# Kernel optimization log

Measured on AMD Instinct MI355X. Metric: run time of the kernel, lower is better.

## Reference

```python
import jax, jax.numpy as jnp
import numpy as np

NODE_DIM = 16
N_VERTS = 54
SEAT_DIM = 4
HIDDEN = 128
N = 16384
EPS = 1e-5


def _layer_norm(x, g, b):
    m = jnp.mean(x, axis=-1, keepdims=True)
    v = jnp.var(x, axis=-1, keepdims=True)
    return (x - m) * jax.lax.rsqrt(v + EPS) * g + b


def setup_inputs() -> dict:
    key = jax.random.key(0)
    ks = jax.random.split(key, 32)
    h = HIDDEN
    mlp_in = h * 3 + 8
    d = {
        "X": jax.random.normal(ks[0], (N, N_VERTS, NODE_DIM), dtype=jnp.float32),
        "A_hat": jax.random.uniform(ks[1], (N_VERTS, N_VERTS), dtype=jnp.float32) / N_VERTS,
        "v1_idx": jax.random.randint(ks[2], (N,), 0, N_VERTS),
        "v2_idx": jax.random.randint(ks[3], (N,), 0, N_VERTS),
        "seat": jax.random.randint(ks[4], (N,), 0, SEAT_DIM),
        # conv layer 0: in NODE_DIM -> h
        "conv0_W": jax.random.normal(ks[5], (NODE_DIM, h), dtype=jnp.float32) * 0.1,
        "conv0_b": jnp.zeros((h,), jnp.float32),
        "ln0_g": jnp.ones((h,), jnp.float32),
        "ln0_b": jnp.zeros((h,), jnp.float32),
        # conv layers 1,2: h -> h
        "conv1_W": jax.random.normal(ks[6], (h, h), dtype=jnp.float32) * 0.05,
        "conv1_b": jnp.zeros((h,), jnp.float32),
        "ln1_g": jnp.ones((h,), jnp.float32),
        "ln1_b": jnp.zeros((h,), jnp.float32),
        "conv2_W": jax.random.normal(ks[7], (h, h), dtype=jnp.float32) * 0.05,
        "conv2_b": jnp.zeros((h,), jnp.float32),
        "ln2_g": jnp.ones((h,), jnp.float32),
        "ln2_b": jnp.zeros((h,), jnp.float32),
        "seat_emb": jax.random.normal(ks[8], (SEAT_DIM + 1, 8), dtype=jnp.float32),
        "mlp_W1": jax.random.normal(ks[9], (mlp_in, 128), dtype=jnp.float32) * 0.05,
        "mlp_b1": jnp.zeros((128,), jnp.float32),
        "mlp_W2": jax.random.normal(ks[10], (128, 64), dtype=jnp.float32) * 0.1,
        "mlp_b2": jnp.zeros((64,), jnp.float32),
        "mlp_W3": jax.random.normal(ks[11], (64, 1), dtype=jnp.float32) * 0.1,
        "mlp_b3": jnp.zeros((1,), jnp.float32),
        # rank head: mlp_in -> 64 -> 1 (sigmoid)
        "rank_W1": jax.random.normal(ks[12], (mlp_in, 64), dtype=jnp.float32) * 0.05,
        "rank_b1": jnp.zeros((64,), jnp.float32),
        "rank_W2": jax.random.normal(ks[13], (64, 1), dtype=jnp.float32) * 0.1,
        "rank_b2": jnp.zeros((1,), jnp.float32),
    }
    return d


def reference(X, A_hat, v1_idx, v2_idx, seat,
              conv0_W, conv0_b, ln0_g, ln0_b,
              conv1_W, conv1_b, ln1_g, ln1_b,
              conv2_W, conv2_b, ln2_g, ln2_b,
              seat_emb,
              mlp_W1, mlp_b1, mlp_W2, mlp_b2, mlp_W3, mlp_b3,
              rank_W1, rank_b1, rank_W2, rank_b2):
    convs = [(conv0_W, conv0_b, ln0_g, ln0_b),
             (conv1_W, conv1_b, ln1_g, ln1_b),
             (conv2_W, conv2_b, ln2_g, ln2_b)]
    H = X  # (N, 54, in_dim)
    for i, (W, b, g, beta) in enumerate(convs):
        HW = jnp.einsum('nvd,dk->nvk', H, W) + b          # linear
        out = jnp.einsum('ij,njk->nik', A_hat, HW)         # adjacency mix
        H_new = jax.nn.relu(_layer_norm(out, g, beta))     # dropout = identity (eval)
        H = H + H_new if i > 0 else H_new
    n = H.shape[0]
    rows = jnp.arange(n)
    v1_emb = H[rows, v1_idx]                               # (N, h)
    v2_emb = H[rows, v2_idx]
    gpool = jnp.mean(H, axis=1)                            # (N, h)
    s_emb = seat_emb[jnp.clip(seat, 0, SEAT_DIM - 1)]      # (N, 8)
    h = jnp.concatenate([v1_emb, v2_emb, gpool, s_emb], axis=-1)
    z = jax.nn.relu(h @ mlp_W1 + mlp_b1)
    z = jax.nn.relu(z @ mlp_W2 + mlp_b2)
    win_logit = z @ mlp_W3 + mlp_b3                        # (N, 1)
    r = jax.nn.relu(h @ rank_W1 + rank_b1)
    rank_pred = jax.nn.sigmoid(r @ rank_W2 + rank_b2)      # (N, 1)
    return (win_logit, rank_pred)
```

## Files before the change

### kernel.cpp

```cpp
#include <hip/hip_runtime.h>
#include <hip/hip_bf16.h>
#include <math.h>


typedef __bf16 bf16x8 __attribute__((ext_vector_type(8)));
typedef float  f32x4  __attribute__((ext_vector_type(4)));
typedef unsigned int u32x4 __attribute__((ext_vector_type(4)));
typedef unsigned int u32x2 __attribute__((ext_vector_type(2)));

#define DEVINL __device__ __forceinline__
#define HROW 400

DEVINL unsigned bfr(float x) {
    unsigned u = __float_as_uint(x);
    return (u + 0x7fffu + ((u >> 16) & 1u)) >> 16;
}
DEVINL unsigned pk2(float a, float b) {
    float2 f; f.x = a; f.y = b;
    __hip_bfloat162 h = __float22bfloat162_rn(f);
    unsigned u;
    __builtin_memcpy(&u, &h, sizeof(u));
    return u;
}
DEVINL unsigned short bf1(float x) {
    return (unsigned short)bfr(x);
}

DEVINL f32x4 MFMA(u32x4 a, u32x4 b, f32x4 c) {
    return __builtin_amdgcn_mfma_f32_16x16x32_bf16(
        __builtin_bit_cast(bf16x8, a), __builtin_bit_cast(bf16x8, b), c, 0, 0, 0);
}

#define TS 36
#define HS 68
DEVINL int TROW(int r) { return r * TS + ((r >> 3) & 1) * 4; }

DEVINL void conv12g(f32x4 (&rg)[8], const unsigned* Hlds,
                    const u32x4* __restrict__ Wp, int w, int g, int c15, int l)
{
    #pragma unroll
    for (int i = 0; i < 8; ++i) rg[i] = (f32x4){0.f, 0.f, 0.f, 0.f};
    #pragma unroll
    for (int ks = 0; ks < 4; ++ks) {
        u32x4 wf0 = Wp[((2 * w + 0) * 4 + ks) * 64 + l];
        u32x4 wf1 = Wp[((2 * w + 1) * 4 + ks) * 64 + l];
        u32x4 hb[4];
        #pragma unroll
        for (int ut = 0; ut < 4; ++ut)
            hb[ut] = *(const u32x4*)&Hlds[(ut * 16 + c15) * HS + ks * 16 + g * 4];
        #pragma unroll
        for (int ut = 0; ut < 4; ++ut) {
            rg[ut]     = MFMA(wf0, hb[ut], rg[ut]);
            rg[4 + ut] = MFMA(wf1, hb[ut], rg[4 + ut]);
        }
    }
}

DEVINL void conv_epi(const f32x4 (&rg)[8], unsigned short* TldsH,
                     const f32x4 (&bb)[2], int w, int g, int c15)
{
    #pragma unroll
    for (int m2 = 0; m2 < 2; ++m2) {
        const int chb = (2 * w + m2) * 16;
        #pragma unroll
        for (int ut = 0; ut < 4; ++ut) {
            const int u = ut * 16 + c15;
            #pragma unroll
            for (int r = 0; r < 4; ++r)
                TldsH[TROW(chb + g * 4 + r) * 2 + u] = bf1(rg[m2 * 4 + ut][r] + bb[m2][r]);
        }
    }
}

DEVINL void do_mix(f32x4 (&rg)[8], const unsigned* Tlds,
                   u32x4 bfA0, u32x4 bfA1, int g, int c15)
{
    #pragma unroll
    for (int mt = 0; mt < 8; ++mt) {
        const int crow = TROW(mt * 16 + c15) + g * 4;
        u32x4 a0 = *(const u32x4*)&Tlds[crow];
        u32x4 a1 = *(const u32x4*)&Tlds[crow + 16];
        f32x4 a = {0.f, 0.f, 0.f, 0.f};
        a = MFMA(a0, bfA0, a);
        a = MFMA(a1, bfA1, a);
        rg[mt] = a;
    }
}

DEVINL void mix_epi(const f32x4 (&rg)[8], float (&Rf)[8][4], unsigned* Hlds,
                    const float* gam, const float* bet, bool resid, bool writeH,
                    int w, int g, int c15)
{
    float s = 0.f, q = 0.f;
    #pragma unroll
    for (int mt = 0; mt < 8; ++mt)
        #pragma unroll
        for (int r = 0; r < 4; ++r) { float x = rg[mt][r]; s += x; q = fmaf(x, x, q); }
    s += __shfl_xor(s, 16); s += __shfl_xor(s, 32);
    q += __shfl_xor(q, 16); q += __shfl_xor(q, 32);
    const float m   = s * (1.f / 128.f);
    const float var = q * (1.f / 128.f) - m * m;
    const float rs  = rsqrtf(var + 1e-5f);
    const int v = w * 16 + c15;
    #pragma unroll
    for (int mt = 0; mt < 8; ++mt) {
        f32x4 gc = *(const f32x4*)&gam[mt * 16 + g * 4];
        f32x4 bc = *(const f32x4*)&bet[mt * 16 + g * 4];
        #pragma unroll
        for (int r = 0; r < 4; ++r) {
            float val = fmaxf((rg[mt][r] - m) * rs * gc[r] + bc[r], 0.f);
            if (resid) val += Rf[mt][r];
            Rf[mt][r] = val;
        }
        if (writeH) {
            u32x2 pr;
            pr[0] = pk2(Rf[mt][0], Rf[mt][1]);
            pr[1] = pk2(Rf[mt][2], Rf[mt][3]);
            *(u32x2*)&Hlds[v * HS + mt * 8 + g * 2] = pr;
        }
    }
}

__global__ __launch_bounds__(256, 4) void gcn_mfma(
    const float* __restrict__ X, const unsigned* __restrict__ AmG,
    const int* __restrict__ v1i, const int* __restrict__ v2i, const int* __restrict__ seat,
    const float* __restrict__ W0, const float* __restrict__ b0v,
    const float* __restrict__ g0v, const float* __restrict__ be0,
    const unsigned* __restrict__ W1G, const float* __restrict__ b1v,
    const float* __restrict__ g1v, const float* __restrict__ be1,
    const unsigned* __restrict__ W2G, const float* __restrict__ b2v,
    const float* __restrict__ g2v, const float* __restrict__ be2,
    const float* __restrict__ semb, float* __restrict__ hws, int spb)
{
    __shared__ unsigned Tlds[128 * TS + 4];
    __shared__ unsigned Hlds[64 * HS];
    __shared__ float    Gb[6][128];
    __shared__ unsigned long long WpS[2];

    float* SmF = (float*)Tlds;

    const int tid = threadIdx.x;
    const int l = tid & 63, w = tid >> 6, g = l >> 4, c15 = l & 15;

    if (tid < 128) {
        const int c = tid;
        Gb[0][c] = g0v[c]; Gb[1][c] = g1v[c]; Gb[2][c] = g2v[c];
        Gb[3][c] = be0[c]; Gb[4][c] = be1[c]; Gb[5][c] = be2[c];
    }
    if (tid == 0) {
        WpS[0] = (unsigned long long)W1G;
        WpS[1] = (unsigned long long)W2G;
    }

    u32x4 W0f[2];
    #pragma unroll
    for (int m2 = 0; m2 < 2; ++m2) {
        const int ch = (2 * w + m2) * 16 + c15;
        unsigned t0[4];
        #pragma unroll
        for (int jj = 0; jj < 4; ++jj) {
            const int k = g * 8 + 2 * jj;
            t0[jj] = (g < 2) ? pk2(W0[k * 128 + ch], W0[(k + 1) * 128 + ch]) : 0u;
        }
        W0f[m2] = (u32x4){t0[0], t0[1], t0[2], t0[3]};
    }
    f32x4 Bv[3][2];
    #pragma unroll
    for (int m2 = 0; m2 < 2; ++m2) {
        const int ch4 = (2 * w + m2) * 16 + g * 4;
        Bv[0][m2] = *(const f32x4*)&b0v[ch4];
        Bv[1][m2] = *(const f32x4*)&b1v[ch4];
        Bv[2][m2] = *(const f32x4*)&b2v[ch4];
    }
    const u32x4* AmG4 = (const u32x4*)AmG;
    u32x4 AmF0 = AmG4[(w * 2 + 0) * 64 + l];
    u32x4 AmF1 = AmG4[(w * 2 + 1) * 64 + l];
    __syncthreads();

    float Rf[8][4];
    f32x4 rg[8];

    #pragma unroll 1
    for (int it = 0; it < spb; ++it) {
        const int n = blockIdx.x + gridDim.x * it;

        const u32x4* W1p = (const u32x4*)(((volatile unsigned long long*)WpS)[0]);
        const u32x4* W2p = (const u32x4*)(((volatile unsigned long long*)WpS)[1]);

        #pragma unroll
        for (int i = 0; i < 8; ++i) rg[i] = (f32x4){0.f, 0.f, 0.f, 0.f};
        #pragma unroll
        for (int ut = 0; ut < 4; ++ut) {
            const int u = ut * 16 + c15;
            u32x4 xb = (u32x4){0u, 0u, 0u, 0u};
            if (g < 2 && u < 54) {
                const f32x4* xp = (const f32x4*)(X + (size_t)n * 864 + u * 16 + g * 8);
                f32x4 f0 = xp[0], f1 = xp[1];
                xb = (u32x4){pk2(f0[0], f0[1]), pk2(f0[2], f0[3]),
                             pk2(f1[0], f1[1]), pk2(f1[2], f1[3])};
            }
            #pragma unroll
            for (int m2 = 0; m2 < 2; ++m2)
                rg[m2 * 4 + ut] = MFMA(W0f[m2], xb, rg[m2 * 4 + ut]);
        }
        conv_epi(rg, (unsigned short*)Tlds, Bv[0], w, g, c15);
        __syncthreads();
        do_mix(rg, Tlds, AmF0, AmF1, g, c15);
        mix_epi(rg, Rf, Hlds, &Gb[0][0], &Gb[3][0], false, true, w, g, c15);
        __syncthreads();

        conv12g(rg, Hlds, W1p, w, g, c15, l);
        conv_epi(rg, (unsigned short*)Tlds, Bv[1], w, g, c15);
        __syncthreads();
        do_mix(rg, Tlds, AmF0, AmF1, g, c15);
        mix_epi(rg, Rf, Hlds, &Gb[1][0], &Gb[4][0], true, true, w, g, c15);
        __syncthreads();

        conv12g(rg, Hlds, W2p, w, g, c15, l);
        conv_epi(rg, (unsigned short*)Tlds, Bv[2], w, g, c15);
        __syncthreads();
        do_mix(rg, Tlds, AmF0, AmF1, g, c15);
        mix_epi(rg, Rf, Hlds, &Gb[2][0], &Gb[5][0], true, true, w, g, c15);
        __syncthreads();

        const int v1 = v1i[n], v2 = v2i[n];
        int st = seat[n];
        st = st < 0 ? 0 : (st > 3 ? 3 : st);
        float* hr = hws + (size_t)n * HROW;
        const int v = w * 16 + c15;

        if (v == v1 || v == v2) {
            #pragma unroll
            for (int mt = 0; mt < 8; ++mt) {
                f32x4 t;
                #pragma unroll
                for (int r = 0; r < 4; ++r) t[r] = Rf[mt][r];
                if (v == v1) *(f32x4*)&hr[mt * 16 + g * 4] = t;
                if (v == v2) *(f32x4*)&hr[128 + mt * 16 + g * 4] = t;
            }
        }

        {
            const int pair = tid & 63;
            const int nv = (w == 3) ? 6 : 16;
            float s0 = 0.f, s1 = 0.f;
            const unsigned* hb = &Hlds[(w * 16) * HS + pair];
            for (int r = 0; r < nv; ++r) {
                const unsigned u = hb[r * HS];
                s0 += __uint_as_float(u << 16);
                s1 += __uint_as_float(u & 0xffff0000u);
            }
            SmF[w * 128 + 2 * pair]     = s0;
            SmF[w * 128 + 2 * pair + 1] = s1;
        }
        __syncthreads();
        if (tid < 128) {
            const float mn = (SmF[tid] + SmF[128 + tid] + SmF[256 + tid] + SmF[384 + tid])
                             * (1.f / 54.f);
            hr[256 + tid] = mn;
        }
        if (tid < 8)       hr[384 + tid] = semb[st * 8 + tid];
        else if (tid < 16) hr[384 + tid] = 0.f;
        __syncthreads();
    }
}

__global__ void head_frag_init(const float* __restrict__ mW1,
                               const float* __restrict__ rW1,
                               const float* __restrict__ mW2,
                               const float* __restrict__ W1t,
                               const float* __restrict__ W2t,
                               const float* __restrict__ Amat,
                               unsigned* __restrict__ W1h, unsigned* __restrict__ W1l,
                               unsigned* __restrict__ R1h, unsigned* __restrict__ W2h,
                               unsigned* __restrict__ W1G, unsigned* __restrict__ W2G,
                               unsigned* __restrict__ AmG)
{
    const int t = blockIdx.x * 256 + threadIdx.x;
    if (t < 13 * 128 * 16) {
        const int j = t & 3, g = (t >> 2) & 3, col = (t >> 4) & 127, ks = t >> 11;
        const int k = ks * 32 + g * 8 + 2 * j;
        const float w0 = (k < 392)     ? mW1[k * 128 + col]       : 0.f;
        const float w1 = (k + 1 < 392) ? mW1[(k + 1) * 128 + col] : 0.f;
        const unsigned h0 = bfr(w0), h1 = bfr(w1);
        const float l0 = w0 - __uint_as_float(h0 << 16);
        const float l1 = w1 - __uint_as_float(h1 << 16);
        const int idx = ((ks * 8 + (col >> 4)) * 64 + g * 16 + (col & 15)) * 4 + j;
        W1h[idx] = h0 | (h1 << 16);
        W1l[idx] = pk2(l0, l1);
    }
    if (t < 13 * 64 * 16) {
        const int j = t & 3, g = (t >> 2) & 3, col = (t >> 4) & 63, ks = t >> 10;
        const int k = ks * 32 + g * 8 + 2 * j;
        const float w0 = (k < 392)     ? rW1[k * 64 + col]       : 0.f;
        const float w1 = (k + 1 < 392) ? rW1[(k + 1) * 64 + col] : 0.f;
        const int idx = ((ks * 4 + (col >> 4)) * 64 + g * 16 + (col & 15)) * 4 + j;
        R1h[idx] = pk2(w0, w1);
    }
    if (t < 4 * 64 * 16) {
        const int j = t & 3, g = (t >> 2) & 3, col = (t >> 4) & 63, ks2 = t >> 10;
        const int k = ks2 * 32 + g * 8 + 2 * j;
        const int idx = ((ks2 * 4 + (col >> 4)) * 64 + g * 16 + (col & 15)) * 4 + j;
        W2h[idx] = pk2(mW2[k * 64 + col], mW2[(k + 1) * 64 + col]);
    }
    if (t < 8 * 4 * 64 * 4) {
        const int j = t & 3, lane = (t >> 2) & 63, ks = (t >> 8) & 3, ct = t >> 10;
        const int g2 = lane >> 4, c15 = lane & 15;
        const int k = ks * 32 + g2 * 8 + 2 * j;
        const int ch = ct * 16 + c15;
        W1G[t] = pk2(W1t[k * 128 + ch], W1t[(k + 1) * 128 + ch]);
        W2G[t] = pk2(W2t[k * 128 + ch], W2t[(k + 1) * 128 + ch]);
    }
    if (t < 2048) {
        const int j = t & 3, lane = (t >> 2) & 63, h = (t >> 8) & 1, wt = t >> 9;
        const int g2 = lane >> 4, cc = lane & 15;
        const int v = wt * 16 + cc;
        const int u = h * 32 + g2 * 8 + 2 * j;
        const float a0 = (v < 54 && u < 54)     ? Amat[v * 54 + u]     : 0.f;
        const float a1 = (v < 54 && u + 1 < 54) ? Amat[v * 54 + u + 1] : 0.f;
        AmG[t] = pk2(a0, a1);
    }
}

__global__ __launch_bounds__(256, 2) void head_mfma(
    const float* __restrict__ hws,
    const unsigned* __restrict__ W1hG, const unsigned* __restrict__ W1lG,
    const unsigned* __restrict__ R1hG, const unsigned* __restrict__ W2hG,
    const float* __restrict__ mb1, const float* __restrict__ mb2,
    const float* __restrict__ mW3, const float* __restrict__ mb3,
    const float* __restrict__ rb1, const float* __restrict__ rW2,
    const float* __restrict__ rb2,
    float* __restrict__ out, int N)
{
    __shared__ u32x4 Zh[16 * 64];

    const int tid = threadIdx.x, l = tid & 63, w = tid >> 6, g = l >> 4, c15 = l & 15;
    const int row = blockIdx.x * 64 + w * 16 + c15;

    const u32x4* W1h4 = (const u32x4*)W1hG;
    const u32x4* W1l4 = (const u32x4*)W1lG;
    const u32x4* R1h4 = (const u32x4*)R1hG;
    const u32x4* W2h4 = (const u32x4*)W2hG;

    f32x4 z1[8], rr[4];
    #pragma unroll
    for (int i = 0; i < 8; ++i) z1[i] = (f32x4){0.f, 0.f, 0.f, 0.f};
    #pragma unroll
    for (int i = 0; i < 4; ++i) rr[i] = (f32x4){0.f, 0.f, 0.f, 0.f};

    #pragma unroll 1
    for (int ks = 0; ks < 13; ++ks) {
        const float* hp = hws + (size_t)row * HROW + ks * 32 + g * 8;
        f32x4 f0 = *(const f32x4*)hp, f1 = *(const f32x4*)(hp + 4);
        float vv[8] = {f0[0], f0[1], f0[2], f0[3], f1[0], f1[1], f1[2], f1[3]};
        unsigned th[4], tl[4];
        #pragma unroll
        for (int jj = 0; jj < 4; ++jj) {
            unsigned ha = bfr(vv[2 * jj]), hb = bfr(vv[2 * jj + 1]);
            th[jj] = ha | (hb << 16);
            tl[jj] = pk2(vv[2 * jj] - __uint_as_float(ha << 16),
                         vv[2 * jj + 1] - __uint_as_float(hb << 16));
        }
        u32x4 ah = (u32x4){th[0], th[1], th[2], th[3]};
        u32x4 al = (u32x4){tl[0], tl[1], tl[2], tl[3]};
        #pragma unroll
        for (int nt = 0; nt < 8; ++nt) {
            u32x4 bh = W1h4[(ks * 8 + nt) * 64 + l];
            u32x4 bl = W1l4[(ks * 8 + nt) * 64 + l];
            f32x4 a = z1[nt];
            a = MFMA(ah, bh, a); a = MFMA(ah, bl, a); a = MFMA(al, bh, a);
            z1[nt] = a;
        }
        #pragma unroll
        for (int nt = 0; nt < 4; ++nt)
            rr[nt] = MFMA(ah, R1h4[(ks * 4 + nt) * 64 + l], rr[nt]);
    }

    float rp[4] = {0.f, 0.f, 0.f, 0.f};
    #pragma unroll
    for (int nt = 0; nt < 4; ++nt) {
        int c = nt * 16 + c15;
        float rb = rb1[c], rw = rW2[c];
        #pragma unroll
        for (int r = 0; r < 4; ++r) rp[r] += fmaxf(rr[nt][r] + rb, 0.f) * rw;
    }
    #pragma unroll
    for (int r = 0; r < 4; ++r) {
        float p = rp[r];
        #pragma unroll
        for (int m = 1; m <= 8; m <<= 1) p += __shfl_xor(p, m);
        if (c15 == 0) {
            int orow = blockIdx.x * 64 + w * 16 + g * 4 + r;
            out[N + orow] = 1.f / (1.f + expf(-(p + rb2[0])));
        }
    }

    {
        unsigned short* zp = (unsigned short*)Zh;
        #pragma unroll
        for (int nt = 0; nt < 8; ++nt) {
            int c = nt * 16 + c15;
            float bb = mb1[c];
            #pragma unroll
            for (int r = 0; r < 4; ++r) {
                float v = fmaxf(z1[nt][r] + bb, 0.f);
                int lanep = ((nt * 2 + (c15 >> 3)) & 3) * 16 + g * 4 + r;
                zp[((w * 4 + (nt >> 1)) * 64 + lanep) * 8 + (c15 & 7)] = (unsigned short)bfr(v);
            }
        }
    }
    __syncthreads();

    f32x4 z2a[4];
    #pragma unroll
    for (int i = 0; i < 4; ++i) z2a[i] = (f32x4){0.f, 0.f, 0.f, 0.f};
    #pragma unroll
    for (int ks2 = 0; ks2 < 4; ++ks2) {
        u32x4 za = Zh[(w * 4 + ks2) * 64 + l];
        #pragma unroll
        for (int nt2 = 0; nt2 < 4; ++nt2)
            z2a[nt2] = MFMA(za, W2h4[(ks2 * 4 + nt2) * 64 + l], z2a[nt2]);
    }
    float wp[4] = {0.f, 0.f, 0.f, 0.f};
    #pragma unroll
    for (int nt2 = 0; nt2 < 4; ++nt2) {
        int c = nt2 * 16 + c15;
        float bb = mb2[c], w3 = mW3[c];
        #pragma unroll
        for (int r = 0; r < 4; ++r) wp[r] += fmaxf(z2a[nt2][r] + bb, 0.f) * w3;
    }
    #pragma unroll
    for (int r = 0; r < 4; ++r) {
        float p = wp[r];
        #pragma unroll
        for (int m = 1; m <= 8; m <<= 1) p += __shfl_xor(p, m);
        if (c15 == 0) {
            int orow = blockIdx.x * 64 + w * 16 + g * 4 + r;
            out[orow] = p + mb3[0];
        }
    }
}

extern "C" void kernel_launch(void* const* d_in, const int* in_sizes, int n_in,
                              void* d_out, int out_size, void* d_ws, size_t ws_size,
                              hipStream_t stream) {
    const float* X        = (const float*)d_in[0];
    const float* A        = (const float*)d_in[1];
    const int*   v1_idx   = (const int*)d_in[2];
    const int*   v2_idx   = (const int*)d_in[3];
    const int*   seat     = (const int*)d_in[4];
    const float* W0       = (const float*)d_in[5];
    const float* b0       = (const float*)d_in[6];
    const float* g0       = (const float*)d_in[7];
    const float* be0      = (const float*)d_in[8];
    const float* W1       = (const float*)d_in[9];
    const float* b1       = (const float*)d_in[10];
    const float* g1       = (const float*)d_in[11];
    const float* be1      = (const float*)d_in[12];
    const float* W2       = (const float*)d_in[13];
    const float* b2       = (const float*)d_in[14];
    const float* g2       = (const float*)d_in[15];
    const float* be2      = (const float*)d_in[16];
    const float* seat_emb = (const float*)d_in[17];
    const float* mW1      = (const float*)d_in[18];
    const float* mb1      = (const float*)d_in[19];
    const float* mW2      = (const float*)d_in[20];
    const float* mb2      = (const float*)d_in[21];
    const float* mW3      = (const float*)d_in[22];
    const float* mb3      = (const float*)d_in[23];
    const float* rW1      = (const float*)d_in[24];
    const float* rb1      = (const float*)d_in[25];
    const float* rW2      = (const float*)d_in[26];
    const float* rb2      = (const float*)d_in[27];

    const int N = in_sizes[2];
    float* out = (float*)d_out;

    float*    hws = (float*)d_ws;
    unsigned* W1h = (unsigned*)((char*)d_ws + (size_t)N * HROW * 4);
    unsigned* W1l = W1h + 26624;
    unsigned* R1h = W1l + 26624;
    unsigned* W2h = R1h + 13312;
    unsigned* W1G = W2h + 4096;
    unsigned* W2G = W1G + 8192;
    unsigned* AmG = W2G + 8192;

    head_frag_init<<<104, 256, 0, stream>>>(mW1, rW1, mW2, W1, W2, A,
                                            W1h, W1l, R1h, W2h, W1G, W2G, AmG);

    const int spb = 8;
    const int gridA = N / spb;
    gcn_mfma<<<gridA, 256, 0, stream>>>(
        X, AmG, v1_idx, v2_idx, seat,
        W0, b0, g0, be0, W1G, b1, g1, be1, W2G, b2, g2, be2,
        seat_emb, hws, spb);

    const int gridB = N / 64;
    head_mfma<<<gridB, 256, 0, stream>>>(
        hws, W1h, W1l, R1h, W2h,
        mb1, mb2, mW3, mb3, rb1, rW2, rb2, out, N);
}
```

Measured before the change: 389.1 us.

## Keep residual in bf16 LDS instead of registers and prepack conv0 weights

Drops the per-thread fp32 residual array Rf[8][4] and instead reads the previous layer's activation back from the bf16 H buffer in LDS for the residual add. The v1/v2 embedding rows are then gathered from LDS. Conv0 weights are prepacked into MFMA fragment layout by the init kernel and loaded each iteration, and biases move to LDS. The T/H padding scheme changes (TROW swizzle removed, HS 68->66). The aim is to cut VGPR pressure and raise occupancy, at the cost of extra LDS traffic, possible bank conflicts, and bf16 rounding of the residual stream, which also feeds the stored embeddings.

```diff
diff --git a/kernel.cpp b/kernel.cpp
--- a/kernel.cpp
+++ b/kernel.cpp
@@ -22,9 +22,9 @@
     __builtin_memcpy(&u, &h, sizeof(u));
     return u;
 }
-DEVINL unsigned short bf1(float x) {
-    return (unsigned short)bfr(x);
-}
+DEVINL unsigned short bf1(float x) { return (unsigned short)bfr(x); }
+DEVINL float lo16(unsigned u) { return __uint_as_float(u << 16); }
+DEVINL float hi16(unsigned u) { return __uint_as_float(u & 0xffff0000u); }
 
 DEVINL f32x4 MFMA(u32x4 a, u32x4 b, f32x4 c) {
     return __builtin_amdgcn_mfma_f32_16x16x32_bf16(
@@ -32,8 +32,7 @@
 }
 
 #define TS 36
-#define HS 68
-DEVINL int TROW(int r) { return r * TS + ((r >> 3) & 1) * 4; }
+#define HS 66
 
 DEVINL void conv12g(f32x4 (&rg)[8], const unsigned* Hlds,
                     const u32x4* __restrict__ Wp, int w, int g, int c15, int l)
@@ -56,18 +55,19 @@
     }
 }
 
-DEVINL void conv_epi(const f32x4 (&rg)[8], unsigned short* TldsH,
-                     const f32x4 (&bb)[2], int w, int g, int c15)
+DEVINL void conv_epi(const f32x4 (&rg)[8], unsigned short* TldsH, const float* bias,
+                     int w, int g, int c15)
 {
     #pragma unroll
     for (int m2 = 0; m2 < 2; ++m2) {
         const int chb = (2 * w + m2) * 16;
+        f32x4 bb = *(const f32x4*)&bias[chb + g * 4];
         #pragma unroll
         for (int ut = 0; ut < 4; ++ut) {
             const int u = ut * 16 + c15;
             #pragma unroll
             for (int r = 0; r < 4; ++r)
-                TldsH[TROW(chb + g * 4 + r) * 2 + u] = bf1(rg[m2 * 4 + ut][r] + bb[m2][r]);
+                TldsH[(chb + g * 4 + r) * (TS * 2) + u] = bf1(rg[m2 * 4 + ut][r] + bb[r]);
         }
     }
 }
@@ -77,7 +77,7 @@
 {
     #pragma unroll
     for (int mt = 0; mt < 8; ++mt) {
-        const int crow = TROW(mt * 16 + c15) + g * 4;
+        const int crow = (mt * 16 + c15) * TS + g * 4;
         u32x4 a0 = *(const u32x4*)&Tlds[crow];
         u32x4 a1 = *(const u32x4*)&Tlds[crow + 16];
         f32x4 a = {0.f, 0.f, 0.f, 0.f};
@@ -87,8 +87,8 @@
     }
 }
 
-DEVINL void mix_epi(const f32x4 (&rg)[8], float (&Rf)[8][4], unsigned* Hlds,
-                    const float* gam, const float* bet, bool resid, bool writeH,
+DEVINL void mix_epi(const f32x4 (&rg)[8], unsigned* Hlds,
+                    const float* gam, const float* bet, bool resid,
                     int w, int g, int c15)
 {
     float s = 0.f, q = 0.f;
@@ -106,25 +106,27 @@
     for (int mt = 0; mt < 8; ++mt) {
         f32x4 gc = *(const f32x4*)&gam[mt * 16 + g * 4];
         f32x4 bc = *(const f32x4*)&bet[mt * 16 + g * 4];
-        #pragma unroll
-        for (int r = 0; r < 4; ++r) {
-            float val = fmaxf((rg[mt][r] - m) * rs * gc[r] + bc[r], 0.f);
-            if (resid) val += Rf[mt][r];
-            Rf[mt][r] = val;
-        }
-        if (writeH) {
-            u32x2 pr;
-            pr[0] = pk2(Rf[mt][0], Rf[mt][1]);
-            pr[1] = pk2(Rf[mt][2], Rf[mt][3]);
-            *(u32x2*)&Hlds[v * HS + mt * 8 + g * 2] = pr;
-        }
+        unsigned* hp = &Hlds[v * HS + mt * 8 + g * 2];
+        float val[4];
+        #pragma unroll
+        for (int r = 0; r < 4; ++r)
+            val[r] = fmaxf((rg[mt][r] - m) * rs * gc[r] + bc[r], 0.f);
+        if (resid) {
+            u32x2 old = *(const u32x2*)hp;
+            val[0] += lo16(old[0]); val[1] += hi16(old[0]);
+            val[2] += lo16(old[1]); val[3] += hi16(old[1]);
+        }
+        u32x2 pr;
+        pr[0] = pk2(val[0], val[1]);
+        pr[1] = pk2(val[2], val[3]);
+        *(u32x2*)hp = pr;
     }
 }
 
 __global__ __launch_bounds__(256, 4) void gcn_mfma(
     const float* __restrict__ X, const unsigned* __restrict__ AmG,
     const int* __restrict__ v1i, const int* __restrict__ v2i, const int* __restrict__ seat,
-    const float* __restrict__ W0, const float* __restrict__ b0v,
+    const unsigned* __restrict__ W0G, const float* __restrict__ b0v,
     const float* __restrict__ g0v, const float* __restrict__ be0,
     const unsigned* __restrict__ W1G, const float* __restrict__ b1v,
     const float* __restrict__ g1v, const float* __restrict__ be1,
@@ -132,10 +134,10 @@
     const float* __restrict__ g2v, const float* __restrict__ be2,
     const float* __restrict__ semb, float* __restrict__ hws, int spb)
 {
-    __shared__ unsigned Tlds[128 * TS + 4];
+    __shared__ unsigned Tlds[128 * TS];
     __shared__ unsigned Hlds[64 * HS];
-    __shared__ float    Gb[6][128];
-    __shared__ unsigned long long WpS[2];
+    __shared__ float    PrmL[9][128];
+    __shared__ unsigned long long WpS[3];
 
     float* SmF = (float*)Tlds;
 
@@ -144,40 +146,20 @@
 
     if (tid < 128) {
         const int c = tid;
-        Gb[0][c] = g0v[c]; Gb[1][c] = g1v[c]; Gb[2][c] = g2v[c];
-        Gb[3][c] = be0[c]; Gb[4][c] = be1[c]; Gb[5][c] = be2[c];
+        PrmL[0][c] = b0v[c]; PrmL[1][c] = b1v[c]; PrmL[2][c] = b2v[c];
+        PrmL[3][c] = g0v[c]; PrmL[4][c] = g1v[c]; PrmL[5][c] = g2v[c];
+        PrmL[6][c] = be0[c]; PrmL[7][c] = be1[c]; PrmL[8][c] = be2[c];
     }
     if (tid == 0) {
         WpS[0] = (unsigned long long)W1G;
         WpS[1] = (unsigned long long)W2G;
-    }
-
-    u32x4 W0f[2];
-    #pragma unroll
-    for (int m2 = 0; m2 < 2; ++m2) {
-        const int ch = (2 * w + m2) * 16 + c15;
-        unsigned t0[4];
-        #pragma unroll
-        for (int jj = 0; jj < 4; ++jj) {
-            const int k = g * 8 + 2 * jj;
-            t0[jj] = (g < 2) ? pk2(W0[k * 128 + ch], W0[(k + 1) * 128 + ch]) : 0u;
-        }
-        W0f[m2] = (u32x4){t0[0], t0[1], t0[2], t0[3]};
-    }
-    f32x4 Bv[3][2];
-    #pragma unroll
-    for (int m2 = 0; m2 < 2; ++m2) {
-        const int ch4 = (2 * w + m2) * 16 + g * 4;
-        Bv[0][m2] = *(const f32x4*)&b0v[ch4];
-        Bv[1][m2] = *(const f32x4*)&b1v[ch4];
-        Bv[2][m2] = *(const f32x4*)&b2v[ch4];
+        WpS[2] = (unsigned long long)W0G;
     }
     const u32x4* AmG4 = (const u32x4*)AmG;
     u32x4 AmF0 = AmG4[(w * 2 + 0) * 64 + l];
     u32x4 AmF1 = AmG4[(w * 2 + 1) * 64 + l];
     __syncthreads();
 
-    float Rf[8][4];
     f32x4 rg[8];
 
     #pragma unroll 1
@@ -186,58 +168,58 @@
 
         const u32x4* W1p = (const u32x4*)(((volatile unsigned long long*)WpS)[0]);
         const u32x4* W2p = (const u32x4*)(((volatile unsigned long long*)WpS)[1]);
-
-        #pragma unroll
-        for (int i = 0; i < 8; ++i) rg[i] = (f32x4){0.f, 0.f, 0.f, 0.f};
-        #pragma unroll
-        for (int ut = 0; ut < 4; ++ut) {
-            const int u = ut * 16 + c15;
-            u32x4 xb = (u32x4){0u, 0u, 0u, 0u};
-            if (g < 2 && u < 54) {
-                const f32x4* xp = (const f32x4*)(X + (size_t)n * 864 + u * 16 + g * 8);
-                f32x4 f0 = xp[0], f1 = xp[1];
-                xb = (u32x4){pk2(f0[0], f0[1]), pk2(f0[2], f0[3]),
-                             pk2(f1[0], f1[1]), pk2(f1[2], f1[3])};
+        const u32x4* W0p = (const u32x4*)(((volatile unsigned long long*)WpS)[2]);
+
+        {
+            u32x4 w0a = W0p[(2 * w + 0) * 64 + l];
+            u32x4 w0b = W0p[(2 * w + 1) * 64 + l];
+            #pragma unroll
+            for (int i = 0; i < 8; ++i) rg[i] = (f32x4){0.f, 0.f, 0.f, 0.f};
+            #pragma unroll
+            for (int ut = 0; ut < 4; ++ut) {
+                const int u = ut * 16 + c15;
+                u32x4 xb = (u32x4){0u, 0u, 0u, 0u};
+                if (g < 2 && u < 54) {
+                    const f32x4* xp = (const f32x4*)(X + (size_t)n * 864 + u * 16 + g * 8);
+                    f32x4 f0 = xp[0], f1 = xp[1];
+                    xb = (u32x4){pk2(f0[0], f0[1]), pk2(f0[2], f0[3]),
+                                 pk2(f1[0], f1[1]), pk2(f1[2], f1[3])};
+                }
+                rg[ut]     = MFMA(w0a, xb, rg[ut]);
+                rg[4 + ut] = MFMA(w0b, xb, rg[4 + ut]);
             }
-            #pragma unroll
-            for (int m2 = 0; m2 < 2; ++m2)
-                rg[m2 * 4 + ut] = MFMA(W0f[m2], xb, rg[m2 * 4 + ut]);
-        }
-        conv_epi(rg, (unsigned short*)Tlds, Bv[0], w, g, c15);
+        }
+        conv_epi(rg, (unsigned short*)Tlds, &PrmL[0][0], w, g, c15);
         __syncthreads();
         do_mix(rg, Tlds, AmF0, AmF1, g, c15);
-        mix_epi(rg, Rf, Hlds, &Gb[0][0], &Gb[3][0], false, true, w, g, c15);
+        mix_epi(rg, Hlds, &PrmL[3][0], &PrmL[6][0], false, w, g, c15);
         __syncthreads();
 
         conv12g(rg, Hlds, W1p, w, g, c15, l);
-        conv_epi(rg, (unsigned short*)Tlds, Bv[1], w, g, c15);
+        conv_epi(rg, (unsigned short*)Tlds, &PrmL[1][0], w, g, c15);
         __syncthreads();
         do_mix(rg, Tlds, AmF0, AmF1, g, c15);
-        mix_epi(rg, Rf, Hlds, &Gb[1][0], &Gb[4][0], true, true, w, g, c15);
+        mix_epi(rg, Hlds, &PrmL[4][0], &PrmL[7][0], true, w, g, c15);
         __syncthreads();
 
         conv12g(rg, Hlds, W2p, w, g, c15, l);
-        conv_epi(rg, (unsigned short*)Tlds, Bv[2], w, g, c15);
+        conv_epi(rg, (unsigned short*)Tlds, &PrmL[2][0], w, g, c15);
         __syncthreads();
         do_mix(rg, Tlds, AmF0, AmF1, g, c15);
-        mix_epi(rg, Rf, Hlds, &Gb[2][0], &Gb[5][0], true, true, w, g, c15);
+        mix_epi(rg, Hlds, &PrmL[5][0], &PrmL[8][0], true, w, g, c15);
         __syncthreads();
 
         const int v1 = v1i[n], v2 = v2i[n];
         int st = seat[n];
         st = st < 0 ? 0 : (st > 3 ? 3 : st);
         float* hr = hws + (size_t)n * HROW;
-        const int v = w * 16 + c15;
-
-        if (v == v1 || v == v2) {
-            #pragma unroll
-            for (int mt = 0; mt < 8; ++mt) {
-                f32x4 t;
-                #pragma unroll
-                for (int r = 0; r < 4; ++r) t[r] = Rf[mt][r];
-                if (v == v1) *(f32x4*)&hr[mt * 16 + g * 4] = t;
-                if (v == v2) *(f32x4*)&hr[128 + mt * 16 + g * 4] = t;
-            }
+
+        if (tid < 128) {
+            const int c = tid;
+            const unsigned u1 = Hlds[v1 * HS + (c >> 1)];
+            const unsigned u2 = Hlds[v2 * HS + (c >> 1)];
+            hr[c]       = (c & 1) ? hi16(u1) : lo16(u1);
+            hr[128 + c] = (c & 1) ? hi16(u2) : lo16(u2);
         }
 
         {
@@ -247,8 +229,8 @@
             const unsigned* hb = &Hlds[(w * 16) * HS + pair];
             for (int r = 0; r < nv; ++r) {
                 const unsigned u = hb[r * HS];
-                s0 += __uint_as_float(u << 16);
-                s1 += __uint_as_float(u & 0xffff0000u);
+                s0 += lo16(u);
+                s1 += hi16(u);
             }
             SmF[w * 128 + 2 * pair]     = s0;
             SmF[w * 128 + 2 * pair + 1] = s1;
@@ -268,13 +250,14 @@
 __global__ void head_frag_init(const float* __restrict__ mW1,
                                const float* __restrict__ rW1,
                                const float* __restrict__ mW2,
+                               const float* __restrict__ W0t,
                                const float* __restrict__ W1t,
                                const float* __restrict__ W2t,
                                const float* __restrict__ Amat,
                                unsigned* __restrict__ W1h, unsigned* __restrict__ W1l,
                                unsigned* __restrict__ R1h, unsigned* __restrict__ W2h,
                                unsigned* __restrict__ W1G, unsigned* __restrict__ W2G,
-                               unsigned* __restrict__ AmG)
+                               unsigned* __restrict__ AmG, unsigned* __restrict__ W0G)
 {
     const int t = blockIdx.x * 256 + threadIdx.x;
     if (t < 13 * 128 * 16) {
@@ -319,6 +302,13 @@
         const float a0 = (v < 54 && u < 54)     ? Amat[v * 54 + u]     : 0.f;
         const float a1 = (v < 54 && u + 1 < 54) ? Amat[v * 54 + u + 1] : 0.f;
         AmG[t] = pk2(a0, a1);
+    }
+    if (t < 2048) {
+        const int j = t & 3, lane = (t >> 2) & 63, ct = t >> 8;
+        const int g2 = lane >> 4, c15 = lane & 15;
+        const int k = g2 * 8 + 2 * j;
+        const int ch = ct * 16 + c15;
+        W0G[t] = (g2 < 2) ? pk2(W0t[k * 128 + ch], W0t[(k + 1) * 128 + ch]) : 0u;
     }
 }
 
@@ -484,15 +474,16 @@
     unsigned* W1G = W2h + 4096;
     unsigned* W2G = W1G + 8192;
     unsigned* AmG = W2G + 8192;
-
-    head_frag_init<<<104, 256, 0, stream>>>(mW1, rW1, mW2, W1, W2, A,
-                                            W1h, W1l, R1h, W2h, W1G, W2G, AmG);
+    unsigned* W0G = AmG + 2048;
+
+    head_frag_init<<<104, 256, 0, stream>>>(mW1, rW1, mW2, W0, W1, W2, A,
+                                            W1h, W1l, R1h, W2h, W1G, W2G, AmG, W0G);
 
     const int spb = 8;
     const int gridA = N / spb;
     gcn_mfma<<<gridA, 256, 0, stream>>>(
         X, AmG, v1_idx, v2_idx, seat,
-        W0, b0, g0, be0, W1G, b1, g1, be1, W2G, b2, g2, be2,
+        W0G, b0, g0, be0, W1G, b1, g1, be1, W2G, b2, g2, be2,
         seat_emb, hws, spb);
 
     const int gridB = N / 64;
```

Result: slower. 466.9 us (+20.0%).
